# Kernel optimization log

Hardware: AMD Instinct MI355X
Metric: run time of the kernel (lower is better)

The kernel has to match this reference:

```python
import jax, jax.numpy as jnp
import numpy as np

B, T, C, H = 4, 2048, 1024, 16
DH = C // H  # 64


def setup_inputs() -> dict:
    key = jax.random.key(0)
    ks = jax.random.split(key, 9)
    s = 1.0 / np.sqrt(C)
    return {
        "x": jax.random.normal(ks[0], (B, T, C), dtype=jnp.float32),
        "Wq": jax.random.normal(ks[1], (C, C), dtype=jnp.float32) * s,
        "bq": jax.random.normal(ks[2], (C,), dtype=jnp.float32) * 0.01,
        "Wk": jax.random.normal(ks[3], (C, C), dtype=jnp.float32) * s,
        "bk": jax.random.normal(ks[4], (C,), dtype=jnp.float32) * 0.01,
        "Wv": jax.random.normal(ks[5], (C, C), dtype=jnp.float32) * s,
        "bv": jax.random.normal(ks[6], (C,), dtype=jnp.float32) * 0.01,
        "Wo": jax.random.normal(ks[7], (C, C), dtype=jnp.float32) * s,
        "bo": jax.random.normal(ks[8], (C,), dtype=jnp.float32) * 0.01,
    }


def reference(x, Wq, bq, Wk, bk, Wv, bv, Wo, bo):
    b, t, c = x.shape
    # q,k,v: [B, H, T, DH]
    def heads(W, bias):
        return (x @ W.T + bias).reshape(b, t, H, DH).transpose(0, 2, 1, 3)
    q = heads(Wq, bq)
    k = heads(Wk, bk)
    v = heads(Wv, bv)
    scale = 1.0 / np.sqrt(DH)
    att = jnp.einsum('bhqd,bhkd->bhqk', q, k) * scale  # [B,H,T,T]
    # causal mask (is_causal=True)
    causal = jnp.tril(jnp.ones((t, t), dtype=bool))
    att = jnp.where(causal[None, None], att, -jnp.inf)
    att = jax.nn.softmax(att, axis=-1)
    y = jnp.einsum('bhqk,bhkd->bhqd', att, v)  # [B,H,T,DH]
    y = y.transpose(0, 2, 1, 3).reshape(b, t, c)
    return y @ Wo.T + bo
```

## Files before the change

kernel.cpp:

```cpp
#include <hip/hip_runtime.h>


typedef _Float16 fp16x8 __attribute__((ext_vector_type(8)));
typedef _Float16 fp16x4 __attribute__((ext_vector_type(4)));
typedef _Float16 fp16x2 __attribute__((ext_vector_type(2)));
typedef float f32x4 __attribute__((ext_vector_type(4)));

#define LOG2E 1.44269504088896f
#define M_FIX 10.0f
#define RTZ_RECENTER 7.043e-4f

__device__ __forceinline__ void async_ld16(const _Float16* g, _Float16* l) {
  __builtin_amdgcn_global_load_lds(
      (const __attribute__((address_space(1))) void*)g,
      (__attribute__((address_space(3))) void*)l, 16, 0, 0);
}

__global__ __launch_bounds__(256) void cast_all(
    const float* __restrict__ x, const float* __restrict__ wq, const float* __restrict__ wk,
    const float* __restrict__ wv, const float* __restrict__ wo,
    _Float16* __restrict__ xh, _Float16* __restrict__ wcat, _Float16* __restrict__ woh) {
  const int bid = blockIdx.x;
  const float* s;
  _Float16* d;
  int off;
  if (bid < 4096) {
    s = x; d = xh; off = bid * 2048;
  } else {
    const int t = bid - 4096;
    const int wi = t >> 9;
    off = (t & 511) * 2048;
    s = (wi == 0) ? wq : (wi == 1) ? wk : (wi == 2) ? wv : wo;
    d = (wi < 3) ? (wcat + wi * 1048576) : woh;
  }
  const int i = off + threadIdx.x * 8;
  float4 a = *(const float4*)(s + i);
  float4 b = *(const float4*)(s + i + 4);
  fp16x8 h;
  h[0] = (_Float16)a.x; h[1] = (_Float16)a.y; h[2] = (_Float16)a.z; h[3] = (_Float16)a.w;
  h[4] = (_Float16)b.x; h[5] = (_Float16)b.y; h[6] = (_Float16)b.z; h[7] = (_Float16)b.w;
  *(fp16x8*)(d + i) = h;
}

__global__ __launch_bounds__(256) void gemm_qkv(
    const _Float16* __restrict__ A, const _Float16* __restrict__ W,
    const float* __restrict__ bq, const float* __restrict__ bk, const float* __restrict__ bv,
    _Float16* __restrict__ qo, _Float16* __restrict__ ko, _Float16* __restrict__ vo) {
  __shared__ __align__(16) _Float16 smem[16384];
  _Float16* As = smem;
  _Float16* Bs = smem + 4096;
  const int tid = threadIdx.x;
  const int m0 = blockIdx.x * 128;
  const int n0 = blockIdx.y * 128;
  const int w = tid >> 6, lane = tid & 63;
  const int lr = lane & 15, quad = lane >> 4;
  const int wm = (w & 1) * 64, wn = (w >> 1) * 64;

  f32x4 acc[4][4];
#pragma unroll
  for (int i = 0; i < 4; ++i)
#pragma unroll
    for (int j = 0; j < 4; ++j) acc[i][j] = (f32x4){0.f, 0.f, 0.f, 0.f};

  const int sr1 = tid >> 2, sc = (tid & 3) * 8, sr2 = sr1 + 64;
  const _Float16* Ag1 = A + (size_t)(m0 + sr1) * 1024 + sc;
  const _Float16* Ag2 = A + (size_t)(m0 + sr2) * 1024 + sc;
  const _Float16* Bg1 = W + (size_t)(n0 + sr1) * 1024 + sc;
  const _Float16* Bg2 = W + (size_t)(n0 + sr2) * 1024 + sc;
  _Float16* Ad1 = &As[sr1 * 32 + sc];
  _Float16* Ad2 = &As[sr2 * 32 + sc];
  _Float16* Bd1 = &Bs[sr1 * 32 + sc];
  _Float16* Bd2 = &Bs[sr2 * 32 + sc];

  for (int kt = 0; kt < 32; ++kt) {
    const int kk = kt * 32;
    __syncthreads();
    async_ld16(Ag1 + kk, Ad1);
    async_ld16(Ag2 + kk, Ad2);
    async_ld16(Bg1 + kk, Bd1);
    async_ld16(Bg2 + kk, Bd2);
    __syncthreads();
    fp16x8 af[4], bf[4];
#pragma unroll
    for (int i = 0; i < 4; ++i) {
      af[i] = *(const fp16x8*)&As[(wm + i * 16 + lr) * 32 + quad * 8];
      bf[i] = *(const fp16x8*)&Bs[(wn + i * 16 + lr) * 32 + quad * 8];
    }
#pragma unroll
    for (int i = 0; i < 4; ++i)
#pragma unroll
      for (int j = 0; j < 4; ++j)
        acc[i][j] = __builtin_amdgcn_mfma_f32_16x16x32_f16(af[i], bf[j], acc[i][j], 0, 0, 0);
  }

  const int wsel = n0 >> 10;
  const float* bias = (wsel == 0) ? bq : (wsel == 1) ? bk : bv;
  _Float16* dst = (wsel == 0) ? qo : (wsel == 1) ? ko : vo;
  float bv4[4];
#pragma unroll
  for (int j = 0; j < 4; ++j) bv4[j] = bias[(n0 + wn + j * 16 + lr) & 1023];

  __syncthreads();
  _Float16* Tr = smem + w * 4096;
#pragma unroll
  for (int j = 0; j < 4; ++j) {
    const int C = j * 16 + lr, ch = C >> 3, cin = C & 7;
#pragma unroll
    for (int i = 0; i < 4; ++i)
#pragma unroll
      for (int r = 0; r < 4; ++r) {
        const int R = i * 16 + quad * 4 + r;
        Tr[R * 64 + ((ch ^ (R & 7)) << 3) + cin] = (_Float16)(acc[i][j][r] + bv4[j]);
      }
  }
  const int r8 = lane >> 3, c8 = lane & 7;
  const int h = ((n0 + wn) & 1023) >> 6;
#pragma unroll
  for (int ch = 0; ch < 8; ++ch) {
    const int Rl = ch * 8 + r8;
    fp16x8 vv = *(const fp16x8*)&Tr[Rl * 64 + ((c8 ^ r8) << 3)];
    const int m = m0 + wm + Rl;
    const int b = m >> 11, t = m & 2047;
    *(fp16x8*)&dst[((size_t)(b * 16 + h) * 2048 + t) * 64 + c8 * 8] = vv;
  }
}

__global__ __launch_bounds__(256) void gemm_out(
    const _Float16* __restrict__ A, const _Float16* __restrict__ W,
    const float* __restrict__ bo, float* __restrict__ out) {
  __shared__ __align__(16) _Float16 smem[16384];
  _Float16* As = smem;
  _Float16* Bs = smem + 4096;
  const int tid = threadIdx.x;
  const int m0 = blockIdx.x * 128;
  const int n0 = blockIdx.y * 128;
  const int w = tid >> 6, lane = tid & 63;
  const int lr = lane & 15, quad = lane >> 4;
  const int wm = (w & 1) * 64, wn = (w >> 1) * 64;

  f32x4 acc[4][4];
#pragma unroll
  for (int i = 0; i < 4; ++i)
#pragma unroll
    for (int j = 0; j < 4; ++j) acc[i][j] = (f32x4){0.f, 0.f, 0.f, 0.f};

  const int sr1 = tid >> 2, sc = (tid & 3) * 8, sr2 = sr1 + 64;
  const _Float16* Ag1 = A + (size_t)(m0 + sr1) * 1024 + sc;
  const _Float16* Ag2 = A + (size_t)(m0 + sr2) * 1024 + sc;
  const _Float16* Bg1 = W + (size_t)(n0 + sr1) * 1024 + sc;
  const _Float16* Bg2 = W + (size_t)(n0 + sr2) * 1024 + sc;
  _Float16* Ad1 = &As[sr1 * 32 + sc];
  _Float16* Ad2 = &As[sr2 * 32 + sc];
  _Float16* Bd1 = &Bs[sr1 * 32 + sc];
  _Float16* Bd2 = &Bs[sr2 * 32 + sc];

  for (int kt = 0; kt < 32; ++kt) {
    const int kk = kt * 32;
    __syncthreads();
    async_ld16(Ag1 + kk, Ad1);
    async_ld16(Ag2 + kk, Ad2);
    async_ld16(Bg1 + kk, Bd1);
    async_ld16(Bg2 + kk, Bd2);
    __syncthreads();
    fp16x8 af[4], bf[4];
#pragma unroll
    for (int i = 0; i < 4; ++i) {
      af[i] = *(const fp16x8*)&As[(wm + i * 16 + lr) * 32 + quad * 8];
      bf[i] = *(const fp16x8*)&Bs[(wn + i * 16 + lr) * 32 + quad * 8];
    }
#pragma unroll
    for (int i = 0; i < 4; ++i)
#pragma unroll
      for (int j = 0; j < 4; ++j)
        acc[i][j] = __builtin_amdgcn_mfma_f32_16x16x32_f16(af[i], bf[j], acc[i][j], 0, 0, 0);
  }

  float bv4[4];
#pragma unroll
  for (int j = 0; j < 4; ++j) bv4[j] = bo[n0 + wn + j * 16 + lr];

  __syncthreads();
  float* Trf = (float*)smem + w * 2048;
  const int r16 = lane >> 4, c16 = lane & 15;
#pragma unroll
  for (int t2 = 0; t2 < 2; ++t2) {
#pragma unroll
    for (int i2 = 0; i2 < 2; ++i2) {
      const int i = t2 * 2 + i2;
#pragma unroll
      for (int j = 0; j < 4; ++j) {
        const int C = j * 16 + lr, ch = C >> 2, cin = C & 3;
#pragma unroll
        for (int r = 0; r < 4; ++r) {
          const int R = i2 * 16 + quad * 4 + r;
          Trf[R * 64 + ((ch ^ (R & 15)) << 2) + cin] = acc[i][j][r] + bv4[j];
        }
      }
    }
#pragma unroll
    for (int ch4 = 0; ch4 < 8; ++ch4) {
      const int Rl = ch4 * 4 + r16;
      float4 vv = *(const float4*)&Trf[Rl * 64 + ((c16 ^ (Rl & 15)) << 2)];
      *(float4*)&out[(size_t)(m0 + wm + t2 * 32 + Rl) * 1024 + n0 + wn + c16 * 4] = vv;
    }
  }
}

typedef __attribute__((address_space(3))) _Float16 lds_f16;

#define PVSTEP(KCT, OFF0, OFF1, OFF2, OFF3)                                        \
  {                                                                                \
    fp16x4 g0, g1, g2, g3;                                                         \
    asm volatile("ds_read_b64_tr_b16 %0, %1 offset:" OFF0                          \
                 : "=v"(g0) : "v"(vtp) : "memory");                                \
    asm volatile("ds_read_b64_tr_b16 %0, %1 offset:" OFF1                          \
                 : "=v"(g1) : "v"(vtp) : "memory");                                \
    asm volatile("ds_read_b64_tr_b16 %0, %1 offset:" OFF2                          \
                 : "=v"(g2) : "v"(vtp) : "memory");                                \
    asm volatile("ds_read_b64_tr_b16 %0, %1 offset:" OFF3                          \
                 : "=v"(g3) : "v"(vtp) : "memory");                                \
    float p0 = __builtin_amdgcn_exp2f(s[KCT][0]);                                  \
    float p1 = __builtin_amdgcn_exp2f(s[KCT][1]);                                  \
    float p2 = __builtin_amdgcn_exp2f(s[KCT][2]);                                  \
    float p3 = __builtin_amdgcn_exp2f(s[KCT][3]);                                  \
    if (dmask) {                                                                   \
      const int kc0 = kb + KCT * 16 + quad * 4;                                    \
      if (kc0 + 0 > qrow) p0 = 0.f;                                                \
      if (kc0 + 1 > qrow) p1 = 0.f;                                                \
      if (kc0 + 2 > qrow) p2 = 0.f;                                                \
      if (kc0 + 3 > qrow) p3 = 0.f;                                                \
    }                                                                              \
    lp += (p0 + p1) + (p2 + p3);                                                   \
    fp16x2 e0 = __builtin_bit_cast(fp16x2, __builtin_amdgcn_cvt_pkrtz(p0, p1));    \
    fp16x2 e1 = __builtin_bit_cast(fp16x2, __builtin_amdgcn_cvt_pkrtz(p2, p3));    \
    fp16x4 pf;                                                                     \
    pf[0] = e0[0]; pf[1] = e0[1]; pf[2] = e1[0]; pf[3] = e1[1];                    \
    asm volatile("s_waitcnt lgkmcnt(0)" ::: "memory");                             \
    __builtin_amdgcn_sched_barrier(0);                                             \
    __builtin_amdgcn_s_setprio(1);                                                 \
    o[0] = __builtin_amdgcn_mfma_f32_16x16x16f16(g0, pf, o[0], 0, 0, 0);           \
    o[1] = __builtin_amdgcn_mfma_f32_16x16x16f16(g1, pf, o[1], 0, 0, 0);           \
    o[2] = __builtin_amdgcn_mfma_f32_16x16x16f16(g2, pf, o[2], 0, 0, 0);           \
    o[3] = __builtin_amdgcn_mfma_f32_16x16x16f16(g3, pf, o[3], 0, 0, 0);           \
    __builtin_amdgcn_s_setprio(0);                                                 \
  }

__global__ __launch_bounds__(256) void attn(
    const _Float16* __restrict__ q, const _Float16* __restrict__ k,
    const _Float16* __restrict__ v, _Float16* __restrict__ y) {
  __shared__ __align__(16) _Float16 smem[16384];
  _Float16* sm = smem;
  const int tid = threadIdx.x;
  const int w = tid >> 6, lane = tid & 63;
  const int lr = lane & 15, quad = lane >> 4;
  const int lr7 = lr & 7;
  const int bx = blockIdx.y;
  const int bh = blockIdx.x;
  const int b = bh >> 4, h = bh & 15;
  const size_t base = (size_t)bh * 2048 * 64;

  const int mlo = bx * 64 + w * 16;
  const int mhi = (31 - bx) * 64 + w * 16;

  const int kr_a = 2 * w * 8 + (lane >> 3);
  const int ksw = (((lane & 7) ^ (lane >> 3)) << 3);
  const _Float16* kp0 = k + base + (size_t)kr_a * 64 + ksw;
  const _Float16* kp1 = kp0 + 8 * 64;
  const _Float16* vp0 = v + base + (size_t)(lane >> 1) * 64 + w * 16 + (lane & 1) * 8;
  const _Float16* vp1 = vp0 + (size_t)32 * 64;
  const int kdA = 2 * w * 512 + lane * 8, kdB = kdA + 512;
  const int vdA = w * 1024 + lane * 8, vdB = vdA + 512;

  async_ld16(kp0, sm + kdA);
  async_ld16(kp1, sm + kdB);
  async_ld16(vp0, sm + 8192 + vdA);
  async_ld16(vp1, sm + 8192 + vdB);
  kp0 += 4096; kp1 += 4096; vp0 += 4096; vp1 += 4096;

  const _Float16 qs = (_Float16)(0.125f * LOG2E);
  fp16x8 qlo[2], qhi[2];
#pragma unroll
  for (int c = 0; c < 2; ++c) {
    fp16x8 t0 = *(const fp16x8*)(q + base + (size_t)(mlo + lr) * 64 + c * 32 + quad * 8);
    fp16x8 t1 = *(const fp16x8*)(q + base + (size_t)(mhi + lr) * 64 + c * 32 + quad * 8);
#pragma unroll
    for (int i = 0; i < 8; ++i) { t0[i] = t0[i] * qs; t1[i] = t1[i] * qs; }
    qlo[c] = t0; qhi[c] = t1;
  }

  const lds_f16* vbase =
      (const lds_f16*)(smem + 8192 + quad * 64 + (lr >> 2) * 16 + (lr & 3) * 4);

  f32x4 olo[4], ohi[4];
#pragma unroll
  for (int dt = 0; dt < 4; ++dt) {
    olo[dt] = (f32x4){0.f, 0.f, 0.f, 0.f};
    ohi[dt] = (f32x4){0.f, 0.f, 0.f, 0.f};
  }
  float lplo = 0.f, lphi = 0.f;

  const float ci = -M_FIX + RTZ_RECENTER;
  const f32x4 cinit = (f32x4){ci, ci, ci, ci};
  const int ntiles = 32 - bx;
  int bsel = 0;

  for (int kt = 0; kt < ntiles; ++kt) {
    asm volatile("s_waitcnt vmcnt(0) lgkmcnt(0)" ::: "memory");
    __syncthreads();
    if (kt + 1 < ntiles) {
      const int st = bsel ^ 4096;
      async_ld16(kp0, sm + st + kdA);
      async_ld16(kp1, sm + st + kdB);
      async_ld16(vp0, sm + 8192 + st + vdA);
      async_ld16(vp1, sm + 8192 + st + vdB);
      kp0 += 4096; kp1 += 4096; vp0 += 4096; vp1 += 4096;
    }
    const _Float16* KsC = sm + bsel;
    const lds_f16* vtp = vbase + bsel;
    const int kb = kt * 64;

    auto process = [&](const fp16x8 (&qf)[2], f32x4 (&o)[4], float& lp,
                       const int qrow, const bool dmask) {
      f32x4 s[4];
      __builtin_amdgcn_s_setprio(1);
#pragma unroll
      for (int kct = 0; kct < 4; ++kct) {
        fp16x8 kf0 = *(const fp16x8*)&KsC[(kct * 16 + lr) * 64 + ((quad ^ lr7) << 3)];
        fp16x8 kf1 = *(const fp16x8*)&KsC[(kct * 16 + lr) * 64 + (((4 + quad) ^ lr7) << 3)];
        s[kct] = __builtin_amdgcn_mfma_f32_16x16x32_f16(kf0, qf[0], cinit, 0, 0, 0);
        s[kct] = __builtin_amdgcn_mfma_f32_16x16x32_f16(kf1, qf[1], s[kct], 0, 0, 0);
      }
      __builtin_amdgcn_s_setprio(0);
      PVSTEP(0, "0", "2048", "4096", "6144")
      PVSTEP(1, "512", "2560", "4608", "6656")
      PVSTEP(2, "1024", "3072", "5120", "7168")
      PVSTEP(3, "1536", "3584", "5632", "7680")
    };

    process(qhi, ohi, lphi, mhi + lr, kt == ntiles - 1);
    if (kt <= bx) process(qlo, olo, lplo, mlo + lr, kt == bx);
    bsel ^= 4096;
  }

  lplo += __shfl_xor(lplo, 16); lplo += __shfl_xor(lplo, 32);
  lphi += __shfl_xor(lphi, 16); lphi += __shfl_xor(lphi, 32);
  const float ilo = 1.f / lplo, ihi = 1.f / lphi;

  _Float16* yplo = y + ((size_t)(b * 2048 + mlo + lr)) * 1024 + h * 64;
  _Float16* yphi = y + ((size_t)(b * 2048 + mhi + lr)) * 1024 + h * 64;
#pragma unroll
  for (int dt = 0; dt < 4; ++dt) {
    fp16x4 slo4, shi4;
#pragma unroll
    for (int r = 0; r < 4; ++r) {
      slo4[r] = (_Float16)(olo[dt][r] * ilo);
      shi4[r] = (_Float16)(ohi[dt][r] * ihi);
    }
    *(fp16x4*)&yplo[dt * 16 + quad * 4] = slo4;
    *(fp16x4*)&yphi[dt * 16 + quad * 4] = shi4;
  }
}

extern "C" void kernel_launch(void* const* d_in, const int* in_sizes, int n_in,
                              void* d_out, int out_size, void* d_ws, size_t ws_size,
                              hipStream_t stream) {
  const float* x  = (const float*)d_in[0];
  const float* Wq = (const float*)d_in[1];
  const float* bq = (const float*)d_in[2];
  const float* Wk = (const float*)d_in[3];
  const float* bk = (const float*)d_in[4];
  const float* Wv = (const float*)d_in[5];
  const float* bv = (const float*)d_in[6];
  const float* Wo = (const float*)d_in[7];
  const float* bo = (const float*)d_in[8];

  _Float16* ws   = (_Float16*)d_ws;
  _Float16* xh   = ws;
  _Float16* Wcat = xh + 8388608;
  _Float16* Woh  = Wcat + 3145728;
  _Float16* qh   = Woh + 1048576;
  _Float16* kh   = qh + 8388608;
  _Float16* vh   = kh + 8388608;
  _Float16* yh   = xh;

  cast_all<<<6144, 256, 0, stream>>>(x, Wq, Wk, Wv, Wo, xh, Wcat, Woh);
  gemm_qkv<<<dim3(64, 24), 256, 0, stream>>>(xh, Wcat, bq, bk, bv, qh, kh, vh);
  attn<<<dim3(64, 16), 256, 0, stream>>>(qh, kh, vh, yh);
  gemm_out<<<dim3(64, 8), 256, 0, stream>>>(yh, Woh, bo, (float*)d_out);
}
```

Before: 255.7 us.

## Double-buffer LDS tiles in QKV and output GEMMs with async prefetch

Both projection GEMMs now alternate between two LDS buffers. The next K-tile is issued with global_load_lds before the MFMAs on the current tile run, so global memory latency overlaps with compute, and the second barrier per iteration is removed. An explicit s_waitcnt before the single barrier ensures the prefetched tile has landed before it is read. This uses the full 32KB smem that was already allocated and adds no new LDS.

```diff
diff --git a/kernel.cpp b/kernel.cpp
--- a/kernel.cpp
+++ b/kernel.cpp
@@ -47,8 +47,7 @@
     const float* __restrict__ bq, const float* __restrict__ bk, const float* __restrict__ bv,
     _Float16* __restrict__ qo, _Float16* __restrict__ ko, _Float16* __restrict__ vo) {
   __shared__ __align__(16) _Float16 smem[16384];
-  _Float16* As = smem;
-  _Float16* Bs = smem + 4096;
+  _Float16* sm = smem;
   const int tid = threadIdx.x;
   const int m0 = blockIdx.x * 128;
   const int n0 = blockIdx.y * 128;
@@ -67,19 +66,28 @@
   const _Float16* Ag2 = A + (size_t)(m0 + sr2) * 1024 + sc;
   const _Float16* Bg1 = W + (size_t)(n0 + sr1) * 1024 + sc;
   const _Float16* Bg2 = W + (size_t)(n0 + sr2) * 1024 + sc;
-  _Float16* Ad1 = &As[sr1 * 32 + sc];
-  _Float16* Ad2 = &As[sr2 * 32 + sc];
-  _Float16* Bd1 = &Bs[sr1 * 32 + sc];
-  _Float16* Bd2 = &Bs[sr2 * 32 + sc];
-
+  const int adA = sr1 * 32 + sc, adB = sr2 * 32 + sc;
+  const int bdA = 4096 + sr1 * 32 + sc, bdB = 4096 + sr2 * 32 + sc;
+
+  async_ld16(Ag1, sm + adA);
+  async_ld16(Ag2, sm + adB);
+  async_ld16(Bg1, sm + bdA);
+  async_ld16(Bg2, sm + bdB);
+
+  int bsel = 0;
   for (int kt = 0; kt < 32; ++kt) {
-    const int kk = kt * 32;
+    asm volatile("s_waitcnt vmcnt(0) lgkmcnt(0)" ::: "memory");
     __syncthreads();
-    async_ld16(Ag1 + kk, Ad1);
-    async_ld16(Ag2 + kk, Ad2);
-    async_ld16(Bg1 + kk, Bd1);
-    async_ld16(Bg2 + kk, Bd2);
-    __syncthreads();
+    if (kt + 1 < 32) {
+      const int st = bsel ^ 8192;
+      const int kk = (kt + 1) * 32;
+      async_ld16(Ag1 + kk, sm + st + adA);
+      async_ld16(Ag2 + kk, sm + st + adB);
+      async_ld16(Bg1 + kk, sm + st + bdA);
+      async_ld16(Bg2 + kk, sm + st + bdB);
+    }
+    const _Float16* As = sm + bsel;
+    const _Float16* Bs = As + 4096;
     fp16x8 af[4], bf[4];
 #pragma unroll
     for (int i = 0; i < 4; ++i) {
@@ -91,6 +99,7 @@
 #pragma unroll
       for (int j = 0; j < 4; ++j)
         acc[i][j] = __builtin_amdgcn_mfma_f32_16x16x32_f16(af[i], bf[j], acc[i][j], 0, 0, 0);
+    bsel ^= 8192;
   }
 
   const int wsel = n0 >> 10;
@@ -129,8 +138,7 @@
     const _Float16* __restrict__ A, const _Float16* __restrict__ W,
     const float* __restrict__ bo, float* __restrict__ out) {
   __shared__ __align__(16) _Float16 smem[16384];
-  _Float16* As = smem;
-  _Float16* Bs = smem + 4096;
+  _Float16* sm = smem;
   const int tid = threadIdx.x;
   const int m0 = blockIdx.x * 128;
   const int n0 = blockIdx.y * 128;
@@ -149,19 +157,28 @@
   const _Float16* Ag2 = A + (size_t)(m0 + sr2) * 1024 + sc;
   const _Float16* Bg1 = W + (size_t)(n0 + sr1) * 1024 + sc;
   const _Float16* Bg2 = W + (size_t)(n0 + sr2) * 1024 + sc;
-  _Float16* Ad1 = &As[sr1 * 32 + sc];
-  _Float16* Ad2 = &As[sr2 * 32 + sc];
-  _Float16* Bd1 = &Bs[sr1 * 32 + sc];
-  _Float16* Bd2 = &Bs[sr2 * 32 + sc];
-
+  const int adA = sr1 * 32 + sc, adB = sr2 * 32 + sc;
+  const int bdA = 4096 + sr1 * 32 + sc, bdB = 4096 + sr2 * 32 + sc;
+
+  async_ld16(Ag1, sm + adA);
+  async_ld16(Ag2, sm + adB);
+  async_ld16(Bg1, sm + bdA);
+  async_ld16(Bg2, sm + bdB);
+
+  int bsel = 0;
   for (int kt = 0; kt < 32; ++kt) {
-    const int kk = kt * 32;
+    asm volatile("s_waitcnt vmcnt(0) lgkmcnt(0)" ::: "memory");
     __syncthreads();
-    async_ld16(Ag1 + kk, Ad1);
-    async_ld16(Ag2 + kk, Ad2);
-    async_ld16(Bg1 + kk, Bd1);
-    async_ld16(Bg2 + kk, Bd2);
-    __syncthreads();
+    if (kt + 1 < 32) {
+      const int st = bsel ^ 8192;
+      const int kk = (kt + 1) * 32;
+      async_ld16(Ag1 + kk, sm + st + adA);
+      async_ld16(Ag2 + kk, sm + st + adB);
+      async_ld16(Bg1 + kk, sm + st + bdA);
+      async_ld16(Bg2 + kk, sm + st + bdB);
+    }
+    const _Float16* As = sm + bsel;
+    const _Float16* Bs = As + 4096;
     fp16x8 af[4], bf[4];
 #pragma unroll
     for (int i = 0; i < 4; ++i) {
@@ -173,6 +190,7 @@
 #pragma unroll
       for (int j = 0; j < 4; ++j)
         acc[i][j] = __builtin_amdgcn_mfma_f32_16x16x32_f16(af[i], bf[j], acc[i][j], 0, 0, 0);
+    bsel ^= 8192;
   }
 
   float bv4[4];
```

New measurement: 278.3 us. 1.09x slower.
